# Kernel tuning notes

Hardware: AMD Instinct MI355X
Metric: run time of the kernel (lower is better)

## Reference

```python
import jax, jax.numpy as jnp
import numpy as np

B, T, H, D = 4, 4096, 1024, 4  # batch, seq_len, hidden_size, max_depth


def setup_inputs() -> dict:
    key = jax.random.key(0)
    ks = jax.random.split(key, 8)
    s = 1.0 / np.sqrt(H)
    x = jax.random.normal(ks[0], (B, T, H), dtype=jnp.float32)
    state = jax.random.normal(ks[1], (B, D, H), dtype=jnp.float32)
    # time_decay_multi initialized as in the torch module: row d = 0.9**(d+1)
    time_decay_multi = jnp.broadcast_to(
        (0.9 ** jnp.arange(1, D + 1, dtype=jnp.float32))[:, None], (D, H)
    ).astype(jnp.float32)
    Wl = jax.random.uniform(ks[2], (D, H), jnp.float32, -s, s)   # level_selector weight [out=D, in=H]
    bl = jax.random.uniform(ks[3], (D,), jnp.float32, -s, s)
    Wv = jax.random.uniform(ks[4], (H, H), jnp.float32, -s, s)
    Wk = jax.random.uniform(ks[5], (H, H), jnp.float32, -s, s)
    Wr = jax.random.uniform(ks[6], (H, H), jnp.float32, -s, s)
    Wo = jax.random.uniform(ks[7], (H, H), jnp.float32, -s, s)
    return {"x": x, "state": state, "time_decay_multi": time_decay_multi,
            "Wl": Wl, "bl": bl, "Wv": Wv, "Wk": Wk, "Wr": Wr, "Wo": Wo}


def reference(x, state, time_decay_multi, Wl, bl, Wv, Wk, Wr, Wo):
    # Projections (torch Linear: y = x @ W.T)
    v = jnp.einsum('bth,oh->bto', x, Wv)
    k = jnp.einsum('bth,oh->bto', x, Wk)
    r = jax.nn.sigmoid(jnp.einsum('bth,oh->bto', x, Wr))
    level_weights = jax.nn.softmax(jnp.einsum('bth,dh->btd', x, Wl) + bl, axis=-1)  # [B,T,D]

    decay = jnp.exp(-jnp.exp(time_decay_multi))        # [D,H]
    decayed_state0 = state * decay[None]               # [B,D,H] (original state is never updated in the loop)
    kv = k * v                                         # [B,T,H]

    # per-step state for depth d is decayed_state0[b,d] + kv[b,t]; weighted sum over depths:
    weighted = (jnp.einsum('btd,bdh->bth', level_weights, decayed_state0)
                + jnp.sum(level_weights, axis=-1, keepdims=True) * kv)  # [B,T,H]
    o = r * weighted
    output = jnp.einsum('bth,oh->bto', o, Wo)

    # new_state after the loop keeps only the LAST timestep contribution
    new_state = decayed_state0 + kv[:, -1][:, None, :]  # [B,D,H]
    return output, new_state
```

## Files before the change

### kernel.cpp

```cpp
#include <hip/hip_runtime.h>

#define B_ 4
#define T_ 4096
#define H_ 1024
#define D_ 4
#define M_ (B_ * T_)
#define OUT_MAIN (M_ * H_)

#define WS_BUF  0UL
#define WS_WK   33554432UL
#define WS_LGW  41943040UL
#define WS_DEC  42205184UL

typedef __bf16 bf16x8 __attribute__((ext_vector_type(8)));
typedef unsigned short u16x4 __attribute__((ext_vector_type(4)));
typedef float f32x4 __attribute__((ext_vector_type(4)));

__device__ __forceinline__ float b2f(unsigned short u) {
    union { unsigned int i; float f; } c;
    c.i = ((unsigned int)u) << 16;
    return c.f;
}
__device__ __forceinline__ unsigned short f2b(float f) {
    union { float f; unsigned int i; } c;
    c.f = f;
    unsigned int x = c.i;
    unsigned int r = (x + 0x7FFFu + ((x >> 16) & 1u)) >> 16;
    return (unsigned short)r;
}

#define BAR()  asm volatile("s_barrier" ::: "memory")
#define VMCNT0() asm volatile("s_waitcnt vmcnt(0)" ::: "memory")
#define GLLDS(gsrc, ldst)                                                     \
    __builtin_amdgcn_global_load_lds(                                         \
        (const __attribute__((address_space(1))) unsigned int*)(gsrc),        \
        (__attribute__((address_space(3))) unsigned int*)(ldst), 16, 0, 0)

__global__ __launch_bounds__(256) void cvt_k(const float* __restrict__ s,
                                             unsigned short* __restrict__ d, int n4)
{
    int i = blockIdx.x * 256 + threadIdx.x;
    const int str = gridDim.x * 256;
    for (; i < n4; i += str) {
        const f32x4 v = ((const f32x4*)s)[i];
        u16x4 o;
        o[0] = f2b(v[0]); o[1] = f2b(v[1]); o[2] = f2b(v[2]); o[3] = f2b(v[3]);
        ((u16x4*)d)[i] = o;
    }
}

__global__ __launch_bounds__(256) void cvtw_k(
    const float* __restrict__ s0, const float* __restrict__ s1,
    const float* __restrict__ s2, const float* __restrict__ s3,
    unsigned short* __restrict__ d)
{
    const int w = blockIdx.y;
    const float* s = (w == 0) ? s0 : (w == 1) ? s1 : (w == 2) ? s2 : s3;
    const int i = blockIdx.x * 256 + threadIdx.x;
    const f32x4 v = ((const f32x4*)s)[i];
    u16x4 o;
    o[0] = f2b(v[0]); o[1] = f2b(v[1]); o[2] = f2b(v[2]); o[3] = f2b(v[3]);
    ((u16x4*)(d + (size_t)w * (H_ * H_)))[i] = o;
}

template <int EPI>
__global__ __launch_bounds__(512, 2) void gemm8p(
    const unsigned short* __restrict__ A,
    const unsigned short* __restrict__ Wt,
    unsigned short* C,
    float* __restrict__ outf,
    const float* __restrict__ lgw,
    const float* __restrict__ dec)
{
    __shared__ __align__(16) unsigned short As[2 * 256 * 64];
    __shared__ __align__(16) unsigned short Bs[2 * 256 * 64];

    const int tid  = threadIdx.x;
    const int wid  = tid >> 6;
    const int lane = tid & 63;
    const int l15  = lane & 15;
    const int l7   = lane & 7;
    const int wrow = wid >> 2;
    const int wcol = wid & 3;
    const int brow = blockIdx.x * 256;
    const int bcol = blockIdx.y * 256;

    int offA[4], offB[4], dst[4];
#pragma unroll
    for (int i = 0; i < 4; ++i) {
        const int G   = i * 512 + tid;
        const int row = G >> 3;
        const int cg  = (G & 7) ^ (row & 7);
        offA[i] = (brow + row) * 1024 + cg * 8;
        offB[i] = (bcol + row) * 1024 + cg * 8;
        dst[i]  = G * 8;
    }

    int aB[8], bB[4], gx[2];
#pragma unroll
    for (int ks = 0; ks < 2; ++ks) gx[ks] = ((ks * 4 + (lane >> 4)) ^ l7) * 8;
#pragma unroll
    for (int mi = 0; mi < 8; ++mi) aB[mi] = (wrow * 128 + mi * 16 + l15) * 64;
#pragma unroll
    for (int ni = 0; ni < 4; ++ni) bB[ni] = (wcol * 64 + ni * 16 + l15) * 64;

    f32x4 acc[8][4];
#pragma unroll
    for (int i = 0; i < 8; ++i)
#pragma unroll
        for (int j = 0; j < 4; ++j)
            acc[i][j] = (f32x4){0.f, 0.f, 0.f, 0.f};

#pragma unroll
    for (int i = 0; i < 4; ++i) {
        GLLDS(A  + offA[i], As + dst[i]);
        GLLDS(Wt + offB[i], Bs + dst[i]);
    }
    VMCNT0();
    BAR();

#pragma unroll 1
    for (int t = 0; t < 16; ++t) {
        const int cur = (t & 1) * 16384;
        const int nxt = 16384 - cur;
        const int kk  = (t + 1) * 64;
        const bool st = (t < 15);
        bf16x8 aR[4][2], bR[4][2];

#pragma unroll
        for (int mi = 0; mi < 4; ++mi)
#pragma unroll
            for (int ks = 0; ks < 2; ++ks)
                aR[mi][ks] = *(const bf16x8*)&As[cur + aB[mi] + gx[ks]];
#pragma unroll
        for (int ni = 0; ni < 2; ++ni)
#pragma unroll
            for (int ks = 0; ks < 2; ++ks)
                bR[ni][ks] = *(const bf16x8*)&Bs[cur + bB[ni] + gx[ks]];
        if (st) {
            GLLDS(A  + offA[0] + kk, As + nxt + dst[0]);
            GLLDS(A  + offA[1] + kk, As + nxt + dst[1]);
            GLLDS(Wt + offB[0] + kk, Bs + nxt + dst[0]);
        }
        BAR();
        __builtin_amdgcn_s_setprio(1);
#pragma unroll
        for (int mi = 0; mi < 4; ++mi)
#pragma unroll
            for (int ni = 0; ni < 2; ++ni)
#pragma unroll
                for (int ks = 0; ks < 2; ++ks)
                    acc[mi][ni] = __builtin_amdgcn_mfma_f32_16x16x32_bf16(
                        aR[mi][ks], bR[ni][ks], acc[mi][ni], 0, 0, 0);
        __builtin_amdgcn_s_setprio(0);
        BAR();

#pragma unroll
        for (int ni = 2; ni < 4; ++ni)
#pragma unroll
            for (int ks = 0; ks < 2; ++ks)
                bR[ni][ks] = *(const bf16x8*)&Bs[cur + bB[ni] + gx[ks]];
        if (st) {
            GLLDS(A  + offA[2] + kk, As + nxt + dst[2]);
            GLLDS(A  + offA[3] + kk, As + nxt + dst[3]);
            GLLDS(Wt + offB[1] + kk, Bs + nxt + dst[1]);
        }
        BAR();
        __builtin_amdgcn_s_setprio(1);
#pragma unroll
        for (int mi = 0; mi < 4; ++mi)
#pragma unroll
            for (int ni = 2; ni < 4; ++ni)
#pragma unroll
                for (int ks = 0; ks < 2; ++ks)
                    acc[mi][ni] = __builtin_amdgcn_mfma_f32_16x16x32_bf16(
                        aR[mi][ks], bR[ni][ks], acc[mi][ni], 0, 0, 0);
        __builtin_amdgcn_s_setprio(0);
        BAR();

#pragma unroll
        for (int mi = 0; mi < 4; ++mi)
#pragma unroll
            for (int ks = 0; ks < 2; ++ks)
                aR[mi][ks] = *(const bf16x8*)&As[cur + aB[4 + mi] + gx[ks]];
        if (st) {
            GLLDS(Wt + offB[2] + kk, Bs + nxt + dst[2]);
            GLLDS(Wt + offB[3] + kk, Bs + nxt + dst[3]);
        }
        BAR();
        __builtin_amdgcn_s_setprio(1);
#pragma unroll
        for (int mi = 0; mi < 4; ++mi)
#pragma unroll
            for (int ni = 2; ni < 4; ++ni)
#pragma unroll
                for (int ks = 0; ks < 2; ++ks)
                    acc[4 + mi][ni] = __builtin_amdgcn_mfma_f32_16x16x32_bf16(
                        aR[mi][ks], bR[ni][ks], acc[4 + mi][ni], 0, 0, 0);
        __builtin_amdgcn_s_setprio(0);
        BAR();

        __builtin_amdgcn_s_setprio(1);
#pragma unroll
        for (int mi = 0; mi < 4; ++mi)
#pragma unroll
            for (int ni = 0; ni < 2; ++ni)
#pragma unroll
                for (int ks = 0; ks < 2; ++ks)
                    acc[4 + mi][ni] = __builtin_amdgcn_mfma_f32_16x16x32_bf16(
                        aR[mi][ks], bR[ni][ks], acc[4 + mi][ni], 0, 0, 0);
        __builtin_amdgcn_s_setprio(0);
        VMCNT0();
        BAR();
    }

    const int orow0 = brow + wrow * 128;
    const int ocol0 = bcol + wcol * 64;
    const int rbase = (lane >> 4) * 4;
    if (EPI == 0) {
#pragma unroll
        for (int mi = 0; mi < 8; ++mi)
#pragma unroll
            for (int j = 0; j < 4; ++j) {
                const size_t r = (size_t)(orow0 + mi * 16 + rbase + j);
#pragma unroll
                for (int ni = 0; ni < 4; ++ni)
                    C[r * 1024 + (ocol0 + ni * 16 + l15)] = f2b(acc[mi][ni][j]);
            }
    } else if (EPI == 1) {
#pragma unroll
        for (int mi = 0; mi < 8; ++mi)
#pragma unroll
            for (int j = 0; j < 4; ++j) {
                const size_t r = (size_t)(orow0 + mi * 16 + rbase + j);
#pragma unroll
                for (int ni = 0; ni < 4; ++ni) {
                    const size_t idx = r * 1024 + (ocol0 + ni * 16 + l15);
                    C[idx] = f2b(acc[mi][ni][j] * b2f(C[idx]));
                }
            }
    } else if (EPI == 2) {
        const int b = brow >> 12;
        float dcol[4][4];
#pragma unroll
        for (int ni = 0; ni < 4; ++ni)
#pragma unroll
            for (int d = 0; d < 4; ++d)
                dcol[ni][d] = dec[b * (D_ * H_) + d * H_ + (ocol0 + ni * 16 + l15)];
#pragma unroll
        for (int mi = 0; mi < 8; ++mi)
#pragma unroll
            for (int j = 0; j < 4; ++j) {
                const int r = orow0 + mi * 16 + rbase + j;
                const f32x4 lw = *(const f32x4*)(lgw + (size_t)r * 4);
                const float wsum = lw[0] + lw[1] + lw[2] + lw[3];
#pragma unroll
                for (int ni = 0; ni < 4; ++ni) {
                    const size_t idx = (size_t)r * 1024 + (ocol0 + ni * 16 + l15);
                    const float rv = 1.0f / (1.0f + __expf(-acc[mi][ni][j]));
                    const float w  = lw[0] * dcol[ni][0] + lw[1] * dcol[ni][1]
                                   + lw[2] * dcol[ni][2] + lw[3] * dcol[ni][3]
                                   + wsum * b2f(C[idx]);
                    C[idx] = f2b(rv * w);
                }
            }
    } else {
#pragma unroll
        for (int mi = 0; mi < 8; ++mi)
#pragma unroll
            for (int j = 0; j < 4; ++j) {
                const size_t r = (size_t)(orow0 + mi * 16 + rbase + j);
#pragma unroll
                for (int ni = 0; ni < 4; ++ni)
                    outf[r * 1024 + (ocol0 + ni * 16 + l15)] = acc[mi][ni][j];
            }
    }
}

__global__ __launch_bounds__(256) void logits_k(
    const float* __restrict__ X, const float* __restrict__ Wl,
    const float* __restrict__ bl, float* __restrict__ lgw)
{
    const int wid  = threadIdx.x >> 6;
    const int lane = threadIdx.x & 63;
    const int row  = blockIdx.x * 4 + wid;
    const float* xp = X + (size_t)row * H_;

    float acc[D_] = {0.f, 0.f, 0.f, 0.f};
    for (int h = lane * 4; h < H_; h += 256) {
        const f32x4 xv = *(const f32x4*)(xp + h);
#pragma unroll
        for (int d = 0; d < D_; ++d) {
            const f32x4 wv = *(const f32x4*)(Wl + d * H_ + h);
            acc[d] += xv[0] * wv[0] + xv[1] * wv[1] + xv[2] * wv[2] + xv[3] * wv[3];
        }
    }
#pragma unroll
    for (int off = 32; off; off >>= 1)
#pragma unroll
        for (int d = 0; d < D_; ++d) acc[d] += __shfl_xor(acc[d], off, 64);

    if (lane == 0) {
        float l[D_];
#pragma unroll
        for (int d = 0; d < D_; ++d) l[d] = acc[d] + bl[d];
        const float mx = fmaxf(fmaxf(l[0], l[1]), fmaxf(l[2], l[3]));
        float e[D_], s = 0.f;
#pragma unroll
        for (int d = 0; d < D_; ++d) { e[d] = __expf(l[d] - mx); s += e[d]; }
        const float inv = 1.0f / s;
        f32x4 o;
#pragma unroll
        for (int d = 0; d < D_; ++d) o[d] = e[d] * inv;
        *(f32x4*)(lgw + (size_t)row * 4) = o;
    }
}

__global__ void decstate_k(const float* __restrict__ state,
                           const float* __restrict__ tdm,
                           float* __restrict__ dec)
{
    const int i = blockIdx.x * blockDim.x + threadIdx.x;
    if (i >= B_ * D_ * H_) return;
    const int dh = i & (D_ * H_ - 1);
    dec[i] = state[i] * __expf(-__expf(tdm[dh]));
}

__global__ __launch_bounds__(256) void newstate_k(
    const float* __restrict__ X, const float* __restrict__ Wk,
    const float* __restrict__ Wv, const float* __restrict__ dec,
    float* __restrict__ out2)
{
    const int wid  = threadIdx.x >> 6;
    const int lane = threadIdx.x & 63;
    const int row  = blockIdx.x * 4 + wid;
    const int b    = row >> 10;
    const int h    = row & (H_ - 1);
    const float* xp = X + ((size_t)(b * T_ + (T_ - 1))) * H_;

    float ak = 0.f, av = 0.f;
    for (int j = lane * 4; j < H_; j += 256) {
        const f32x4 xv = *(const f32x4*)(xp + j);
        const f32x4 wk = *(const f32x4*)(Wk + (size_t)h * H_ + j);
        const f32x4 wv = *(const f32x4*)(Wv + (size_t)h * H_ + j);
        ak += xv[0]*wk[0] + xv[1]*wk[1] + xv[2]*wk[2] + xv[3]*wk[3];
        av += xv[0]*wv[0] + xv[1]*wv[1] + xv[2]*wv[2] + xv[3]*wv[3];
    }
#pragma unroll
    for (int off = 32; off; off >>= 1) {
        ak += __shfl_xor(ak, off, 64);
        av += __shfl_xor(av, off, 64);
    }
    if (lane == 0) {
        const float kv = ak * av;
#pragma unroll
        for (int d = 0; d < D_; ++d)
            out2[(size_t)(b * D_ + d) * H_ + h] = dec[(b * D_ + d) * H_ + h] + kv;
    }
}

extern "C" void kernel_launch(void* const* d_in, const int* in_sizes, int n_in,
                              void* d_out, int out_size, void* d_ws, size_t ws_size,
                              hipStream_t stream)
{
    const float* x   = (const float*)d_in[0];
    const float* st  = (const float*)d_in[1];
    const float* tdm = (const float*)d_in[2];
    const float* Wl  = (const float*)d_in[3];
    const float* bl  = (const float*)d_in[4];
    const float* Wv  = (const float*)d_in[5];
    const float* Wk  = (const float*)d_in[6];
    const float* Wr  = (const float*)d_in[7];
    const float* Wo  = (const float*)d_in[8];
    float* out = (float*)d_out;

    char* ws = (char*)d_ws;
    unsigned short* buf  = (unsigned short*)(ws + WS_BUF);
    unsigned short* wk_b = (unsigned short*)(ws + WS_WK);
    unsigned short* wv_b = wk_b + 1 * (H_ * H_);
    unsigned short* wr_b = wk_b + 2 * (H_ * H_);
    unsigned short* wo_b = wk_b + 3 * (H_ * H_);
    float* lgw = (float*)(ws + WS_LGW);
    float* dec = (float*)(ws + WS_DEC);

    unsigned short* xb = (unsigned short*)out;

    logits_k<<<M_ / 4, 256, 0, stream>>>(x, Wl, bl, lgw);
    decstate_k<<<(B_ * D_ * H_ + 255) / 256, 256, 0, stream>>>(st, tdm, dec);
    newstate_k<<<(B_ * H_) / 4, 256, 0, stream>>>(x, Wk, Wv, dec, out + OUT_MAIN);

    cvt_k<<<2048, 256, 0, stream>>>(x, xb, OUT_MAIN / 4);
    cvtw_k<<<dim3(1024, 4), 256, 0, stream>>>(Wk, Wv, Wr, Wo, wk_b);

    const dim3 g(M_ / 256, H_ / 256), blk(512);

    hipLaunchKernelGGL((gemm8p<0>), g, blk, 0, stream, xb, wk_b, buf,
                       (float*)nullptr, (const float*)nullptr, (const float*)nullptr);
    hipLaunchKernelGGL((gemm8p<1>), g, blk, 0, stream, xb, wv_b, buf,
                       (float*)nullptr, (const float*)nullptr, (const float*)nullptr);
    hipLaunchKernelGGL((gemm8p<2>), g, blk, 0, stream, xb, wr_b, buf,
                       (float*)nullptr, (const float*)lgw, (const float*)dec);
    hipLaunchKernelGGL((gemm8p<3>), g, blk, 0, stream, buf, wo_b, (unsigned short*)nullptr,
                       out, (const float*)nullptr, (const float*)nullptr);
}
```

Baseline: 199.4 us.

## Fuse K and V projection GEMMs into one kernel sharing the A tile

Replaces the two separate K and V GEMM launches with one fused kernel. Each block loads one 256-row tile of x and computes both the K and V products against a 128-column slice of each weight, then writes k*v straight out. This removes a full bf16 intermediate write and read-back of k and a second pass over x. In exchange the output tile per block is smaller (128 columns), and the kernel uses a new, more finely interleaved load/MFMA schedule with partial vmcnt waits.

Measured after the change: 192.7 us. -3.3%, faster.

```diff
diff --git a/kernel.cpp b/kernel.cpp
--- a/kernel.cpp
+++ b/kernel.cpp
@@ -30,7 +30,6 @@
 }
 
 #define BAR()  asm volatile("s_barrier" ::: "memory")
-#define VMCNT0() asm volatile("s_waitcnt vmcnt(0)" ::: "memory")
 #define GLLDS(gsrc, ldst)                                                     \
     __builtin_amdgcn_global_load_lds(                                         \
         (const __attribute__((address_space(1))) unsigned int*)(gsrc),        \
@@ -61,6 +60,150 @@
     u16x4 o;
     o[0] = f2b(v[0]); o[1] = f2b(v[1]); o[2] = f2b(v[2]); o[3] = f2b(v[3]);
     ((u16x4*)(d + (size_t)w * (H_ * H_)))[i] = o;
+}
+
+__global__ __launch_bounds__(512, 2) void gemm_kv(
+    const unsigned short* __restrict__ A,
+    const unsigned short* __restrict__ Wk,
+    const unsigned short* __restrict__ Wv,
+    unsigned short* __restrict__ Ckv)
+{
+    __shared__ __align__(16) unsigned short As[2 * 16384];
+    __shared__ __align__(16) unsigned short Bks[2 * 8192];
+    __shared__ __align__(16) unsigned short Bvs[2 * 8192];
+
+    const int tid  = threadIdx.x;
+    const int wid  = tid >> 6;
+    const int lane = tid & 63;
+    const int l15  = lane & 15;
+    const int q    = lane >> 4;
+    const int wrow = wid >> 1;
+    const int wcol = wid & 1;
+    const int brow = blockIdx.x * 256;
+    const int bcol = blockIdx.y * 128;
+
+    int offA[4], dstA[4];
+#pragma unroll
+    for (int i = 0; i < 4; ++i) {
+        const int G   = i * 512 + tid;
+        const int row = G >> 3;
+        const int cg  = (G & 7) ^ (row & 7);
+        offA[i] = (brow + row) * 1024 + cg * 8;
+        dstA[i] = G * 8;
+    }
+    int offB[2], dstB[2];
+#pragma unroll
+    for (int j = 0; j < 2; ++j) {
+        const int G   = j * 512 + tid;
+        const int row = G >> 3;
+        const int cg  = (G & 7) ^ (row & 7);
+        offB[j] = (bcol + row) * 1024 + cg * 8;
+        dstB[j] = G * 8;
+    }
+
+    int gx[2];
+#pragma unroll
+    for (int ks = 0; ks < 2; ++ks) gx[ks] = ((ks * 4 + q) ^ (l15 & 7)) * 8;
+    int aB[4], bB[4];
+#pragma unroll
+    for (int mi = 0; mi < 4; ++mi) aB[mi] = (wrow * 64 + mi * 16 + l15) * 64;
+#pragma unroll
+    for (int ni = 0; ni < 4; ++ni) bB[ni] = (wcol * 64 + ni * 16 + l15) * 64;
+
+    f32x4 accK[4][4], accV[4][4];
+#pragma unroll
+    for (int i = 0; i < 4; ++i)
+#pragma unroll
+        for (int j = 0; j < 4; ++j) {
+            accK[i][j] = (f32x4){0.f, 0.f, 0.f, 0.f};
+            accV[i][j] = (f32x4){0.f, 0.f, 0.f, 0.f};
+        }
+
+#define SGA(bo, tau, i_)  GLLDS(A  + offA[i_] + (tau) * 64, As  + (bo) + dstA[i_])
+#define SGBK(bo, tau, j_) GLLDS(Wk + offB[j_] + (tau) * 64, Bks + (bo) + dstB[j_])
+#define SGBV(bo, tau, j_) GLLDS(Wv + offB[j_] + (tau) * 64, Bvs + (bo) + dstB[j_])
+#define RD_AALL(CUR)                                                          \
+    _Pragma("unroll") for (int mi = 0; mi < 4; ++mi)                          \
+    _Pragma("unroll") for (int ks = 0; ks < 2; ++ks)                          \
+        aR[mi][ks] = *(const bf16x8*)&As[(CUR) + aB[mi] + gx[ks]];
+#define RD_B(ARR, CURB, N0)                                                   \
+    _Pragma("unroll") for (int nj = 0; nj < 2; ++nj)                          \
+    _Pragma("unroll") for (int ks = 0; ks < 2; ++ks)                          \
+        bR[nj][ks] = *(const bf16x8*)&ARR[(CURB) + bB[(N0) + nj] + gx[ks]];
+#define MFMA16(ACC, NB)                                                       \
+    __builtin_amdgcn_s_setprio(1);                                            \
+    _Pragma("unroll") for (int mi = 0; mi < 4; ++mi)                          \
+    _Pragma("unroll") for (int nj = 0; nj < 2; ++nj)                          \
+    _Pragma("unroll") for (int ks = 0; ks < 2; ++ks)                          \
+        ACC[mi][(NB) + nj] = __builtin_amdgcn_mfma_f32_16x16x32_bf16(         \
+            aR[mi][ks], bR[nj][ks], ACC[mi][(NB) + nj], 0, 0, 0);             \
+    __builtin_amdgcn_s_setprio(0);
+
+#pragma unroll
+    for (int i = 0; i < 4; ++i) SGA(0, 0, i);
+    SGBK(0, 0, 0); SGBK(0, 0, 1);
+    SGBV(0, 0, 0); SGBV(0, 0, 1);
+#pragma unroll
+    for (int i = 0; i < 4; ++i) SGA(16384, 1, i);
+    asm volatile("s_waitcnt vmcnt(4)" ::: "memory");
+    BAR();
+
+#pragma unroll 1
+    for (int t = 0; t < 15; ++t) {
+        const int curA = (t & 1) << 14;
+        const int curB = (t & 1) << 13;
+        const int nxtB = curB ^ 8192;
+        bf16x8 aR[4][2], bR[2][2];
+
+        RD_AALL(curA); RD_B(Bks, curB, 0);
+        SGBK(nxtB, t + 1, 0); SGBK(nxtB, t + 1, 1);
+        BAR(); MFMA16(accK, 0); BAR();
+
+        RD_B(Bks, curB, 2);
+        SGBV(nxtB, t + 1, 0); SGBV(nxtB, t + 1, 1);
+        BAR(); MFMA16(accK, 2); BAR();
+
+        RD_B(Bvs, curB, 0);
+        if (t < 14) { SGA(curA, t + 2, 0); SGA(curA, t + 2, 1); }
+        BAR(); MFMA16(accV, 0); BAR();
+
+        RD_B(Bvs, curB, 2);
+        if (t < 14) { SGA(curA, t + 2, 2); SGA(curA, t + 2, 3); }
+        BAR(); MFMA16(accV, 2);
+        if (t < 14) asm volatile("s_waitcnt vmcnt(4)" ::: "memory");
+        else        asm volatile("s_waitcnt vmcnt(0)" ::: "memory");
+        BAR();
+    }
+    {
+        const int curA = 16384, curB = 8192;
+        bf16x8 aR[4][2], bR[2][2];
+        RD_AALL(curA);
+        RD_B(Bks, curB, 0); MFMA16(accK, 0);
+        RD_B(Bks, curB, 2); MFMA16(accK, 2);
+        RD_B(Bvs, curB, 0); MFMA16(accV, 0);
+        RD_B(Bvs, curB, 2); MFMA16(accV, 2);
+    }
+#undef SGA
+#undef SGBK
+#undef SGBV
+#undef RD_AALL
+#undef RD_B
+#undef MFMA16
+
+    const int orow0 = brow + wrow * 64;
+    const int ocol0 = bcol + wcol * 64;
+    const int rbase = q * 4;
+#pragma unroll
+    for (int mi = 0; mi < 4; ++mi)
+#pragma unroll
+        for (int j = 0; j < 4; ++j) {
+            const size_t r = (size_t)(orow0 + mi * 16 + rbase + j);
+#pragma unroll
+            for (int ni = 0; ni < 4; ++ni) {
+                const size_t idx = r * 1024 + (ocol0 + ni * 16 + l15);
+                Ckv[idx] = f2b(accV[mi][ni][j] * b2f(f2b(accK[mi][ni][j])));
+            }
+        }
 }
 
 template <int EPI>
@@ -116,7 +259,7 @@
         GLLDS(A  + offA[i], As + dst[i]);
         GLLDS(Wt + offB[i], Bs + dst[i]);
     }
-    VMCNT0();
+    asm volatile("s_waitcnt vmcnt(0)" ::: "memory");
     BAR();
 
 #pragma unroll 1
@@ -210,36 +353,14 @@
                     acc[4 + mi][ni] = __builtin_amdgcn_mfma_f32_16x16x32_bf16(
                         aR[mi][ks], bR[ni][ks], acc[4 + mi][ni], 0, 0, 0);
         __builtin_amdgcn_s_setprio(0);
-        VMCNT0();
+        asm volatile("s_waitcnt vmcnt(0)" ::: "memory");
         BAR();
     }
 
     const int orow0 = brow + wrow * 128;
     const int ocol0 = bcol + wcol * 64;
     const int rbase = (lane >> 4) * 4;
-    if (EPI == 0) {
-#pragma unroll
-        for (int mi = 0; mi < 8; ++mi)
-#pragma unroll
-            for (int j = 0; j < 4; ++j) {
-                const size_t r = (size_t)(orow0 + mi * 16 + rbase + j);
-#pragma unroll
-                for (int ni = 0; ni < 4; ++ni)
-                    C[r * 1024 + (ocol0 + ni * 16 + l15)] = f2b(acc[mi][ni][j]);
-            }
-    } else if (EPI == 1) {
-#pragma unroll
-        for (int mi = 0; mi < 8; ++mi)
-#pragma unroll
-            for (int j = 0; j < 4; ++j) {
-                const size_t r = (size_t)(orow0 + mi * 16 + rbase + j);
-#pragma unroll
-                for (int ni = 0; ni < 4; ++ni) {
-                    const size_t idx = r * 1024 + (ocol0 + ni * 16 + l15);
-                    C[idx] = f2b(acc[mi][ni][j] * b2f(C[idx]));
-                }
-            }
-    } else if (EPI == 2) {
+    if (EPI == 2) {
         const int b = brow >> 12;
         float dcol[4][4];
 #pragma unroll
@@ -392,12 +513,9 @@
     cvt_k<<<2048, 256, 0, stream>>>(x, xb, OUT_MAIN / 4);
     cvtw_k<<<dim3(1024, 4), 256, 0, stream>>>(Wk, Wv, Wr, Wo, wk_b);
 
+    gemm_kv<<<dim3(M_ / 256, H_ / 128), 512, 0, stream>>>(xb, wk_b, wv_b, buf);
+
     const dim3 g(M_ / 256, H_ / 256), blk(512);
-
-    hipLaunchKernelGGL((gemm8p<0>), g, blk, 0, stream, xb, wk_b, buf,
-                       (float*)nullptr, (const float*)nullptr, (const float*)nullptr);
-    hipLaunchKernelGGL((gemm8p<1>), g, blk, 0, stream, xb, wv_b, buf,
-                       (float*)nullptr, (const float*)nullptr, (const float*)nullptr);
     hipLaunchKernelGGL((gemm8p<2>), g, blk, 0, stream, xb, wr_b, buf,
                        (float*)nullptr, (const float*)lgw, (const float*)dec);
     hipLaunchKernelGGL((gemm8p<3>), g, blk, 0, stream, buf, wo_b, (unsigned short*)nullptr,
```

## Fuse K/V/R projection GEMMs into one kernel and merge logits with x conversion

Applied to the files above, without the earlier changes.

Replaces three separate 256x256-tile GEMMs (K, V, R), which round-tripped intermediates through a bf16 buffer, with one 128x128-tile kernel. It loads each A tile once, multiplies it against all three weight tiles, and applies the gating epilogue in registers. The logits/softmax kernel now also writes the bf16 copy of x, which removes a separate conversion pass. This trades smaller tiles, more LDS and more accumulator registers (possibly lower occupancy) for far less global memory traffic and fewer launches. The epilogue rounds k to bf16 before the multiply to match the previous numerics.

After: 177.0 us. 11.2% less time.

```diff
diff --git a/kernel.cpp b/kernel.cpp
--- a/kernel.cpp
+++ b/kernel.cpp
@@ -30,24 +30,10 @@
 }
 
 #define BAR()  asm volatile("s_barrier" ::: "memory")
-#define VMCNT0() asm volatile("s_waitcnt vmcnt(0)" ::: "memory")
 #define GLLDS(gsrc, ldst)                                                     \
     __builtin_amdgcn_global_load_lds(                                         \
         (const __attribute__((address_space(1))) unsigned int*)(gsrc),        \
         (__attribute__((address_space(3))) unsigned int*)(ldst), 16, 0, 0)
-
-__global__ __launch_bounds__(256) void cvt_k(const float* __restrict__ s,
-                                             unsigned short* __restrict__ d, int n4)
-{
-    int i = blockIdx.x * 256 + threadIdx.x;
-    const int str = gridDim.x * 256;
-    for (; i < n4; i += str) {
-        const f32x4 v = ((const f32x4*)s)[i];
-        u16x4 o;
-        o[0] = f2b(v[0]); o[1] = f2b(v[1]); o[2] = f2b(v[2]); o[3] = f2b(v[3]);
-        ((u16x4*)d)[i] = o;
-    }
-}
 
 __global__ __launch_bounds__(256) void cvtw_k(
     const float* __restrict__ s0, const float* __restrict__ s1,
@@ -63,14 +49,255 @@
     ((u16x4*)(d + (size_t)w * (H_ * H_)))[i] = o;
 }
 
-template <int EPI>
-__global__ __launch_bounds__(512, 2) void gemm8p(
+__global__ __launch_bounds__(256) void logcvt_k(
+    const float* __restrict__ X, const float* __restrict__ Wl,
+    const float* __restrict__ bl, float* __restrict__ lgw,
+    unsigned short* __restrict__ xb)
+{
+    const int wid  = threadIdx.x >> 6;
+    const int lane = threadIdx.x & 63;
+    const int row  = blockIdx.x * 4 + wid;
+    const float* xp = X + (size_t)row * H_;
+    unsigned short* xo = xb + (size_t)row * H_;
+
+    float acc[D_] = {0.f, 0.f, 0.f, 0.f};
+    for (int h = lane * 4; h < H_; h += 256) {
+        const f32x4 xv = *(const f32x4*)(xp + h);
+        u16x4 xc;
+        xc[0] = f2b(xv[0]); xc[1] = f2b(xv[1]);
+        xc[2] = f2b(xv[2]); xc[3] = f2b(xv[3]);
+        *(u16x4*)(xo + h) = xc;
+#pragma unroll
+        for (int d = 0; d < D_; ++d) {
+            const f32x4 wv = *(const f32x4*)(Wl + d * H_ + h);
+            acc[d] += xv[0] * wv[0] + xv[1] * wv[1] + xv[2] * wv[2] + xv[3] * wv[3];
+        }
+    }
+#pragma unroll
+    for (int off = 32; off; off >>= 1)
+#pragma unroll
+        for (int d = 0; d < D_; ++d) acc[d] += __shfl_xor(acc[d], off, 64);
+
+    if (lane == 0) {
+        float l[D_];
+#pragma unroll
+        for (int d = 0; d < D_; ++d) l[d] = acc[d] + bl[d];
+        const float mx = fmaxf(fmaxf(l[0], l[1]), fmaxf(l[2], l[3]));
+        float e[D_], s = 0.f;
+#pragma unroll
+        for (int d = 0; d < D_; ++d) { e[d] = __expf(l[d] - mx); s += e[d]; }
+        const float inv = 1.0f / s;
+        f32x4 o;
+#pragma unroll
+        for (int d = 0; d < D_; ++d) o[d] = e[d] * inv;
+        *(f32x4*)(lgw + (size_t)row * 4) = o;
+    }
+}
+
+__global__ void decstate_k(const float* __restrict__ state,
+                           const float* __restrict__ tdm,
+                           float* __restrict__ dec)
+{
+    const int i = blockIdx.x * blockDim.x + threadIdx.x;
+    if (i >= B_ * D_ * H_) return;
+    const int dh = i & (D_ * H_ - 1);
+    dec[i] = state[i] * __expf(-__expf(tdm[dh]));
+}
+
+__global__ __launch_bounds__(256) void newstate_k(
+    const float* __restrict__ X, const float* __restrict__ Wk,
+    const float* __restrict__ Wv, const float* __restrict__ dec,
+    float* __restrict__ out2)
+{
+    const int wid  = threadIdx.x >> 6;
+    const int lane = threadIdx.x & 63;
+    const int row  = blockIdx.x * 4 + wid;
+    const int b    = row >> 10;
+    const int h    = row & (H_ - 1);
+    const float* xp = X + ((size_t)(b * T_ + (T_ - 1))) * H_;
+
+    float ak = 0.f, av = 0.f;
+    for (int j = lane * 4; j < H_; j += 256) {
+        const f32x4 xv = *(const f32x4*)(xp + j);
+        const f32x4 wk = *(const f32x4*)(Wk + (size_t)h * H_ + j);
+        const f32x4 wv = *(const f32x4*)(Wv + (size_t)h * H_ + j);
+        ak += xv[0]*wk[0] + xv[1]*wk[1] + xv[2]*wk[2] + xv[3]*wk[3];
+        av += xv[0]*wv[0] + xv[1]*wv[1] + xv[2]*wv[2] + xv[3]*wv[3];
+    }
+#pragma unroll
+    for (int off = 32; off; off >>= 1) {
+        ak += __shfl_xor(ak, off, 64);
+        av += __shfl_xor(av, off, 64);
+    }
+    if (lane == 0) {
+        const float kv = ak * av;
+#pragma unroll
+        for (int d = 0; d < D_; ++d)
+            out2[(size_t)(b * D_ + d) * H_ + h] = dec[(b * D_ + d) * H_ + h] + kv;
+    }
+}
+
+__global__ __launch_bounds__(512, 2) void gemm_kvr(
+    const unsigned short* __restrict__ A,
+    const unsigned short* __restrict__ Wk,
+    const unsigned short* __restrict__ Wv,
+    const unsigned short* __restrict__ Wr,
+    unsigned short* __restrict__ Co,
+    const float* __restrict__ lgw,
+    const float* __restrict__ dec)
+{
+    __shared__ __align__(16) unsigned short As [2 * 8192];
+    __shared__ __align__(16) unsigned short Bks[2 * 8192];
+    __shared__ __align__(16) unsigned short Bvs[2 * 8192];
+    __shared__ __align__(16) unsigned short Brs[2 * 8192];
+
+    const int tid  = threadIdx.x;
+    const int wid  = tid >> 6;
+    const int lane = tid & 63;
+    const int l15  = lane & 15;
+    const int q    = lane >> 4;
+    const int wrow = wid >> 2;
+    const int wcol = wid & 3;
+    const int bcol = blockIdx.x * 128;
+    const int brow = blockIdx.y * 128;
+
+    const int g0row = tid >> 3, g0cg = (tid & 7) ^ (g0row & 7);
+    const int g1row = 64 + g0row, g1cg = (tid & 7) ^ (g1row & 7);
+    const int offA0 = (brow + g0row) * 1024 + g0cg * 8;
+    const int offA1 = (brow + g1row) * 1024 + g1cg * 8;
+    const int offB0 = (bcol + g0row) * 1024 + g0cg * 8;
+    const int offB1 = (bcol + g1row) * 1024 + g1cg * 8;
+    const int dst0 = tid * 8;
+    const int dst1 = 4096 + tid * 8;
+
+    int gx[2];
+#pragma unroll
+    for (int ks = 0; ks < 2; ++ks) gx[ks] = ((ks * 4 + q) ^ (l15 & 7)) * 8;
+    int aB[4], bB[2];
+#pragma unroll
+    for (int mi = 0; mi < 4; ++mi) aB[mi] = (wrow * 64 + mi * 16 + l15) * 64;
+#pragma unroll
+    for (int ni = 0; ni < 2; ++ni) bB[ni] = (wcol * 32 + ni * 16 + l15) * 64;
+
+    f32x4 accK[4][2], accV[4][2], accR[4][2];
+#pragma unroll
+    for (int i = 0; i < 4; ++i)
+#pragma unroll
+        for (int j = 0; j < 2; ++j) {
+            accK[i][j] = (f32x4){0.f, 0.f, 0.f, 0.f};
+            accV[i][j] = (f32x4){0.f, 0.f, 0.f, 0.f};
+            accR[i][j] = (f32x4){0.f, 0.f, 0.f, 0.f};
+        }
+
+#define SG_A(bo, tau)  do { GLLDS(A  + offA0 + (tau) * 64, As  + (bo) + dst0); \
+                            GLLDS(A  + offA1 + (tau) * 64, As  + (bo) + dst1); } while (0)
+#define SG_BK(bo, tau) do { GLLDS(Wk + offB0 + (tau) * 64, Bks + (bo) + dst0); \
+                            GLLDS(Wk + offB1 + (tau) * 64, Bks + (bo) + dst1); } while (0)
+#define SG_BV(bo, tau) do { GLLDS(Wv + offB0 + (tau) * 64, Bvs + (bo) + dst0); \
+                            GLLDS(Wv + offB1 + (tau) * 64, Bvs + (bo) + dst1); } while (0)
+#define SG_BR(bo, tau) do { GLLDS(Wr + offB0 + (tau) * 64, Brs + (bo) + dst0); \
+                            GLLDS(Wr + offB1 + (tau) * 64, Brs + (bo) + dst1); } while (0)
+#define RD_AALL(CUR)                                                          \
+    _Pragma("unroll") for (int mi = 0; mi < 4; ++mi)                          \
+    _Pragma("unroll") for (int ks = 0; ks < 2; ++ks)                          \
+        aR[mi][ks] = *(const bf16x8*)&As[(CUR) + aB[mi] + gx[ks]];
+#define RD_B(ARR, CUR)                                                        \
+    _Pragma("unroll") for (int nj = 0; nj < 2; ++nj)                          \
+    _Pragma("unroll") for (int ks = 0; ks < 2; ++ks)                          \
+        bR[nj][ks] = *(const bf16x8*)&ARR[(CUR) + bB[nj] + gx[ks]];
+#define MFMA16(ACC)                                                           \
+    __builtin_amdgcn_s_setprio(1);                                            \
+    _Pragma("unroll") for (int mi = 0; mi < 4; ++mi)                          \
+    _Pragma("unroll") for (int nj = 0; nj < 2; ++nj)                          \
+    _Pragma("unroll") for (int ks = 0; ks < 2; ++ks)                          \
+        ACC[mi][nj] = __builtin_amdgcn_mfma_f32_16x16x32_bf16(                \
+            aR[mi][ks], bR[nj][ks], ACC[mi][nj], 0, 0, 0);                    \
+    __builtin_amdgcn_s_setprio(0);
+
+    SG_A(0, 0); SG_BK(0, 0); SG_BV(0, 0); SG_BR(0, 0);
+    asm volatile("s_waitcnt vmcnt(4)" ::: "memory");
+    BAR();
+
+#pragma unroll 1
+    for (int t = 0; t < 15; ++t) {
+        const int cur = (t & 1) << 13;
+        const int nxt = cur ^ 8192;
+        bf16x8 aR[4][2], bR[2][2];
+
+        RD_AALL(cur); RD_B(Bks, cur);
+        SG_A(nxt, t + 1); SG_BK(nxt, t + 1);
+        BAR(); MFMA16(accK);
+        asm volatile("s_waitcnt vmcnt(6)" ::: "memory");
+        BAR();
+
+        RD_B(Bvs, cur);
+        SG_BV(nxt, t + 1);
+        BAR(); MFMA16(accV);
+        asm volatile("s_waitcnt vmcnt(6)" ::: "memory");
+        BAR();
+
+        RD_B(Brs, cur);
+        SG_BR(nxt, t + 1);
+        BAR(); MFMA16(accR);
+        asm volatile("s_waitcnt vmcnt(4)" ::: "memory");
+        BAR();
+    }
+    {
+        const int cur = 8192;
+        bf16x8 aR[4][2], bR[2][2];
+        RD_AALL(cur); RD_B(Bks, cur);
+        BAR(); MFMA16(accK);
+        asm volatile("s_waitcnt vmcnt(2)" ::: "memory");
+        BAR();
+        RD_B(Bvs, cur);
+        BAR(); MFMA16(accV);
+        asm volatile("s_waitcnt vmcnt(0)" ::: "memory");
+        BAR();
+        RD_B(Brs, cur);
+        MFMA16(accR);
+    }
+#undef SG_A
+#undef SG_BK
+#undef SG_BV
+#undef SG_BR
+#undef RD_AALL
+#undef RD_B
+#undef MFMA16
+
+    const int orow0 = brow + wrow * 64;
+    const int ocol0 = bcol + wcol * 32;
+    const int rbase = q * 4;
+    const int b = brow >> 12;
+    float dcol[2][4];
+#pragma unroll
+    for (int ni = 0; ni < 2; ++ni)
+#pragma unroll
+        for (int d = 0; d < 4; ++d)
+            dcol[ni][d] = dec[b * (D_ * H_) + d * H_ + (ocol0 + ni * 16 + l15)];
+#pragma unroll
+    for (int mi = 0; mi < 4; ++mi)
+#pragma unroll
+        for (int j = 0; j < 4; ++j) {
+            const int r = orow0 + mi * 16 + rbase + j;
+            const f32x4 lw = *(const f32x4*)(lgw + (size_t)r * 4);
+            const float wsum = lw[0] + lw[1] + lw[2] + lw[3];
+#pragma unroll
+            for (int ni = 0; ni < 2; ++ni) {
+                const size_t idx = (size_t)r * 1024 + (ocol0 + ni * 16 + l15);
+                const float kvf = b2f(f2b(accV[mi][ni][j] * b2f(f2b(accK[mi][ni][j]))));
+                const float rv  = 1.0f / (1.0f + __expf(-accR[mi][ni][j]));
+                const float w   = lw[0] * dcol[ni][0] + lw[1] * dcol[ni][1]
+                                + lw[2] * dcol[ni][2] + lw[3] * dcol[ni][3]
+                                + wsum * kvf;
+                Co[idx] = f2b(rv * w);
+            }
+        }
+}
+
+__global__ __launch_bounds__(512, 2) void gemm_o(
     const unsigned short* __restrict__ A,
     const unsigned short* __restrict__ Wt,
-    unsigned short* C,
-    float* __restrict__ outf,
-    const float* __restrict__ lgw,
-    const float* __restrict__ dec)
+    float* __restrict__ outf)
 {
     __shared__ __align__(16) unsigned short As[2 * 256 * 64];
     __shared__ __align__(16) unsigned short Bs[2 * 256 * 64];
@@ -116,7 +343,7 @@
         GLLDS(A  + offA[i], As + dst[i]);
         GLLDS(Wt + offB[i], Bs + dst[i]);
     }
-    VMCNT0();
+    asm volatile("s_waitcnt vmcnt(0)" ::: "memory");
     BAR();
 
 #pragma unroll 1
@@ -210,153 +437,22 @@
                     acc[4 + mi][ni] = __builtin_amdgcn_mfma_f32_16x16x32_bf16(
                         aR[mi][ks], bR[ni][ks], acc[4 + mi][ni], 0, 0, 0);
         __builtin_amdgcn_s_setprio(0);
-        VMCNT0();
+        asm volatile("s_waitcnt vmcnt(0)" ::: "memory");
         BAR();
     }
 
     const int orow0 = brow + wrow * 128;
     const int ocol0 = bcol + wcol * 64;
     const int rbase = (lane >> 4) * 4;
-    if (EPI == 0) {
-#pragma unroll
-        for (int mi = 0; mi < 8; ++mi)
-#pragma unroll
-            for (int j = 0; j < 4; ++j) {
-                const size_t r = (size_t)(orow0 + mi * 16 + rbase + j);
-#pragma unroll
-                for (int ni = 0; ni < 4; ++ni)
-                    C[r * 1024 + (ocol0 + ni * 16 + l15)] = f2b(acc[mi][ni][j]);
-            }
-    } else if (EPI == 1) {
-#pragma unroll
-        for (int mi = 0; mi < 8; ++mi)
-#pragma unroll
-            for (int j = 0; j < 4; ++j) {
-                const size_t r = (size_t)(orow0 + mi * 16 + rbase + j);
-#pragma unroll
-                for (int ni = 0; ni < 4; ++ni) {
-                    const size_t idx = r * 1024 + (ocol0 + ni * 16 + l15);
-                    C[idx] = f2b(acc[mi][ni][j] * b2f(C[idx]));
-                }
-            }
-    } else if (EPI == 2) {
-        const int b = brow >> 12;
-        float dcol[4][4];
-#pragma unroll
-        for (int ni = 0; ni < 4; ++ni)
-#pragma unroll
-            for (int d = 0; d < 4; ++d)
-                dcol[ni][d] = dec[b * (D_ * H_) + d * H_ + (ocol0 + ni * 16 + l15)];
-#pragma unroll
-        for (int mi = 0; mi < 8; ++mi)
-#pragma unroll
-            for (int j = 0; j < 4; ++j) {
-                const int r = orow0 + mi * 16 + rbase + j;
-                const f32x4 lw = *(const f32x4*)(lgw + (size_t)r * 4);
-                const float wsum = lw[0] + lw[1] + lw[2] + lw[3];
-#pragma unroll
-                for (int ni = 0; ni < 4; ++ni) {
-                    const size_t idx = (size_t)r * 1024 + (ocol0 + ni * 16 + l15);
-                    const float rv = 1.0f / (1.0f + __expf(-acc[mi][ni][j]));
-                    const float w  = lw[0] * dcol[ni][0] + lw[1] * dcol[ni][1]
-                                   + lw[2] * dcol[ni][2] + lw[3] * dcol[ni][3]
-                                   + wsum * b2f(C[idx]);
-                    C[idx] = f2b(rv * w);
-                }
-            }
-    } else {
-#pragma unroll
-        for (int mi = 0; mi < 8; ++mi)
-#pragma unroll
-            for (int j = 0; j < 4; ++j) {
-                const size_t r = (size_t)(orow0 + mi * 16 + rbase + j);
-#pragma unroll
-                for (int ni = 0; ni < 4; ++ni)
-                    outf[r * 1024 + (ocol0 + ni * 16 + l15)] = acc[mi][ni][j];
-            }
-    }
-}
-
-__global__ __launch_bounds__(256) void logits_k(
-    const float* __restrict__ X, const float* __restrict__ Wl,
-    const float* __restrict__ bl, float* __restrict__ lgw)
-{
-    const int wid  = threadIdx.x >> 6;
-    const int lane = threadIdx.x & 63;
-    const int row  = blockIdx.x * 4 + wid;
-    const float* xp = X + (size_t)row * H_;
-
-    float acc[D_] = {0.f, 0.f, 0.f, 0.f};
-    for (int h = lane * 4; h < H_; h += 256) {
-        const f32x4 xv = *(const f32x4*)(xp + h);
-#pragma unroll
-        for (int d = 0; d < D_; ++d) {
-            const f32x4 wv = *(const f32x4*)(Wl + d * H_ + h);
-            acc[d] += xv[0] * wv[0] + xv[1] * wv[1] + xv[2] * wv[2] + xv[3] * wv[3];
-        }
-    }
-#pragma unroll
-    for (int off = 32; off; off >>= 1)
-#pragma unroll
-        for (int d = 0; d < D_; ++d) acc[d] += __shfl_xor(acc[d], off, 64);
-
-    if (lane == 0) {
-        float l[D_];
-#pragma unroll
-        for (int d = 0; d < D_; ++d) l[d] = acc[d] + bl[d];
-        const float mx = fmaxf(fmaxf(l[0], l[1]), fmaxf(l[2], l[3]));
-        float e[D_], s = 0.f;
-#pragma unroll
-        for (int d = 0; d < D_; ++d) { e[d] = __expf(l[d] - mx); s += e[d]; }
-        const float inv = 1.0f / s;
-        f32x4 o;
-#pragma unroll
-        for (int d = 0; d < D_; ++d) o[d] = e[d] * inv;
-        *(f32x4*)(lgw + (size_t)row * 4) = o;
-    }
-}
-
-__global__ void decstate_k(const float* __restrict__ state,
-                           const float* __restrict__ tdm,
-                           float* __restrict__ dec)
-{
-    const int i = blockIdx.x * blockDim.x + threadIdx.x;
-    if (i >= B_ * D_ * H_) return;
-    const int dh = i & (D_ * H_ - 1);
-    dec[i] = state[i] * __expf(-__expf(tdm[dh]));
-}
-
-__global__ __launch_bounds__(256) void newstate_k(
-    const float* __restrict__ X, const float* __restrict__ Wk,
-    const float* __restrict__ Wv, const float* __restrict__ dec,
-    float* __restrict__ out2)
-{
-    const int wid  = threadIdx.x >> 6;
-    const int lane = threadIdx.x & 63;
-    const int row  = blockIdx.x * 4 + wid;
-    const int b    = row >> 10;
-    const int h    = row & (H_ - 1);
-    const float* xp = X + ((size_t)(b * T_ + (T_ - 1))) * H_;
-
-    float ak = 0.f, av = 0.f;
-    for (int j = lane * 4; j < H_; j += 256) {
-        const f32x4 xv = *(const f32x4*)(xp + j);
-        const f32x4 wk = *(const f32x4*)(Wk + (size_t)h * H_ + j);
-        const f32x4 wv = *(const f32x4*)(Wv + (size_t)h * H_ + j);
-        ak += xv[0]*wk[0] + xv[1]*wk[1] + xv[2]*wk[2] + xv[3]*wk[3];
-        av += xv[0]*wv[0] + xv[1]*wv[1] + xv[2]*wv[2] + xv[3]*wv[3];
-    }
-#pragma unroll
-    for (int off = 32; off; off >>= 1) {
-        ak += __shfl_xor(ak, off, 64);
-        av += __shfl_xor(av, off, 64);
-    }
-    if (lane == 0) {
-        const float kv = ak * av;
-#pragma unroll
-        for (int d = 0; d < D_; ++d)
-            out2[(size_t)(b * D_ + d) * H_ + h] = dec[(b * D_ + d) * H_ + h] + kv;
-    }
+#pragma unroll
+    for (int mi = 0; mi < 8; ++mi)
+#pragma unroll
+        for (int j = 0; j < 4; ++j) {
+            const size_t r = (size_t)(orow0 + mi * 16 + rbase + j);
+#pragma unroll
+            for (int ni = 0; ni < 4; ++ni)
+                outf[r * 1024 + (ocol0 + ni * 16 + l15)] = acc[mi][ni][j];
+        }
 }
 
 extern "C" void kernel_launch(void* const* d_in, const int* in_sizes, int n_in,
@@ -385,21 +481,13 @@
 
     unsigned short* xb = (unsigned short*)out;
 
-    logits_k<<<M_ / 4, 256, 0, stream>>>(x, Wl, bl, lgw);
     decstate_k<<<(B_ * D_ * H_ + 255) / 256, 256, 0, stream>>>(st, tdm, dec);
+    logcvt_k<<<M_ / 4, 256, 0, stream>>>(x, Wl, bl, lgw, xb);
     newstate_k<<<(B_ * H_) / 4, 256, 0, stream>>>(x, Wk, Wv, dec, out + OUT_MAIN);
-
-    cvt_k<<<2048, 256, 0, stream>>>(x, xb, OUT_MAIN / 4);
     cvtw_k<<<dim3(1024, 4), 256, 0, stream>>>(Wk, Wv, Wr, Wo, wk_b);
 
-    const dim3 g(M_ / 256, H_ / 256), blk(512);
-
-    hipLaunchKernelGGL((gemm8p<0>), g, blk, 0, stream, xb, wk_b, buf,
-                       (float*)nullptr, (const float*)nullptr, (const float*)nullptr);
-    hipLaunchKernelGGL((gemm8p<1>), g, blk, 0, stream, xb, wv_b, buf,
-                       (float*)nullptr, (const float*)nullptr, (const float*)nullptr);
-    hipLaunchKernelGGL((gemm8p<2>), g, blk, 0, stream, xb, wr_b, buf,
-                       (float*)nullptr, (const float*)lgw, (const float*)dec);
-    hipLaunchKernelGGL((gemm8p<3>), g, blk, 0, stream, buf, wo_b, (unsigned short*)nullptr,
-                       out, (const float*)nullptr, (const float*)nullptr);
-}
+    gemm_kvr<<<dim3(H_ / 128, M_ / 128), 512, 0, stream>>>(
+        xb, wk_b, wv_b, wr_b, buf, lgw, dec);
+
+    gemm_o<<<dim3(M_ / 256, H_ / 256), 512, 0, stream>>>(buf, wo_b, out);
+}
```
